# Performance work log

Measured on AMD Instinct MI355X. Metric: run time of the kernel, lower is better.

The kernel has to match this reference:

```python
import jax, jax.numpy as jnp
import numpy as np

B, E, D, P, H = 8192, 100, 300, 100, 20  # batch, experts, embed, projection, hidden

def setup_inputs() -> dict:
    key = jax.random.key(0)
    ks = jax.random.split(key, 10)
    return {
        "x": jax.random.normal(ks[0], (B, D), dtype=jnp.float32),
        "y": jax.random.normal(ks[1], (B, D), dtype=jnp.float32),
        "tag": jax.random.uniform(ks[2], (B, 1), dtype=jnp.float32),
        "weights_1": jax.random.normal(ks[3], (E, D, P), dtype=jnp.float32) * (2.0 / (D + P)) ** 0.5,
        "bias_1": jax.random.normal(ks[4], (E, P), dtype=jnp.float32) * 0.1,
        "hidden_weights": jax.random.normal(ks[5], (E, 2 * P + 2, H), dtype=jnp.float32) * 0.07,
        "hidden_bias": jax.random.normal(ks[6], (E, H), dtype=jnp.float32),
        "outlayer_weights": jax.random.normal(ks[7], (E, H, 1), dtype=jnp.float32) * 0.3,
        "outlayer_bias": jax.random.uniform(ks[8], (E, 1), dtype=jnp.float32),
        "weights_all": jax.random.normal(ks[9], (D, E), dtype=jnp.float32) * (2.0 / (D + E)) ** 0.5,
    }

def reference(x, y, tag, weights_1, bias_1, hidden_weights, hidden_bias,
              outlayer_weights, outlayer_bias, weights_all):
    eps = 1e-8
    # gating: softmax((x+y) @ W_all) over experts  -> [B, E, 1]
    w = jax.nn.softmax((x + y) @ weights_all, axis=1)[:, :, None]
    # per-expert projections: [B, E, P]
    xp = jnp.einsum('bd,edp->bep', x, weights_1) + bias_1
    yp = jnp.einsum('bd,edp->bep', y, weights_1) + bias_1
    # cosine similarity along projection dim (torch semantics: clamp each norm)
    nx = jnp.maximum(jnp.sqrt(jnp.sum(xp * xp, axis=2)), eps)
    ny = jnp.maximum(jnp.sqrt(jnp.sum(yp * yp, axis=2)), eps)
    cos = jnp.sum(xp * yp, axis=2) / (nx * ny)  # [B, E]
    tag_rep = jnp.broadcast_to(tag[:, None, :], (x.shape[0], weights_1.shape[0], tag.shape[1]))
    feat = jnp.concatenate([cos[:, :, None], xp + yp, jnp.abs(xp - yp), tag_rep], axis=2)  # [B,E,2P+2]
    h = jax.nn.relu(jnp.einsum('bef,efh->beh', feat, hidden_weights) + hidden_bias)  # [B,E,H]
    d = jnp.einsum('beh,eho->beo', h, outlayer_weights) + outlayer_bias  # [B,E,1]
    probs = jnp.squeeze(jnp.sum(w * d, axis=1), axis=-1)  # [B]
    return probs
```

## Files before the change

kernel.cpp:

```cpp
#include <hip/hip_runtime.h>
#include <math.h>

#define B_ 8192
#define E_ 100
#define D_ 300
#define P_ 100
#define H_ 20
#define F_ 202
#define NT 10
#define NWG 12800

typedef __attribute__((ext_vector_type(8))) short bf16x8;
typedef __attribute__((ext_vector_type(8))) _Float16 f16x8;
typedef __attribute__((ext_vector_type(4))) float f32x4;
typedef __attribute__((ext_vector_type(8))) unsigned short us8;

#define WG_OFF 0
#define AB_OFF 3276800
#define W1_OFF (AB_OFF + 20971520)
#define PD_OFF (W1_OFF + 14336000)
#define WS_NEEDED (PD_OFF + 3276800)

__device__ __forceinline__ unsigned short f2bf(float f) {
    unsigned int u = __float_as_uint(f);
    u = (u + 0x7FFF + ((u >> 16) & 1)) >> 16;
    return (unsigned short)u;
}
__device__ __forceinline__ float bf2f(unsigned short h) {
    return __uint_as_float(((unsigned int)h) << 16);
}

#define GLOAD16(g, l) \
    __builtin_amdgcn_global_load_lds((const __attribute__((address_space(1))) unsigned int*)(g), \
                                     (__attribute__((address_space(3))) unsigned int*)(l), 16, 0, 0)

__global__ __launch_bounds__(256) void prep_xy(const float* __restrict__ x,
                                               const float* __restrict__ y,
                                               unsigned short* __restrict__ ab2)
{
    const int bi = blockIdx.x;
    const int rb = bi / NT, t = bi - rb * NT;
    for (int s = threadIdx.x; s < 512; s += 256) {
        const int kg = s >> 7, row = s & 127;
        const float* src = ((row < 64) ? x : y) + (size_t)(rb * 64 + (row & 63)) * D_;
        const int k0 = t * 32 + kg * 8;
        us8 hi, lo;
        #pragma unroll
        for (int j = 0; j < 8; ++j) {
            const int k = k0 + j;
            const float v = (k < D_) ? src[k] : 0.f;
            const unsigned short h = f2bf(v);
            hi[j] = h;
            lo[j] = f2bf(v - bf2f(h));
        }
        unsigned short* tb = ab2 + (size_t)bi * 8192;
        *(us8*)(tb + (size_t)s * 8)         = hi;
        *(us8*)(tb + (size_t)(512 + s) * 8) = lo;
    }
}

__global__ __launch_bounds__(256) void prep_w1(const float* __restrict__ w1,
                                               unsigned short* __restrict__ w1b2)
{
    const int bi = blockIdx.x;
    const int e = bi / NT, t = bi - e * NT;
    for (int s = threadIdx.x; s < 448; s += 256) {
        const int kg = s / 112, p = s - kg * 112;
        const int k0 = t * 32 + kg * 8;
        us8 hi, lo;
        #pragma unroll
        for (int j = 0; j < 8; ++j) {
            const int k = k0 + j;
            const float v = (p < P_ && k < D_) ? w1[((size_t)e * D_ + k) * P_ + p] : 0.f;
            const unsigned short h = f2bf(v);
            hi[j] = h;
            lo[j] = f2bf(v - bf2f(h));
        }
        unsigned short* tb = w1b2 + (size_t)bi * 7168;
        *(us8*)(tb + (size_t)s * 8)         = hi;
        *(us8*)(tb + (size_t)(448 + s) * 8) = lo;
    }
}

__global__ __launch_bounds__(128) void gate_kernel(
    const float* __restrict__ x, const float* __restrict__ y,
    const float* __restrict__ wall, float* __restrict__ wgate)
{
    __shared__ float s[D_];
    __shared__ float zv[128];
    __shared__ float red[128];
    const int b = blockIdx.x;
    const int tid = threadIdx.x;

    for (int d = tid; d < D_; d += 128)
        s[d] = x[(size_t)b * D_ + d] + y[(size_t)b * D_ + d];
    __syncthreads();

    float acc = 0.f;
    if (tid < E_)
        for (int d = 0; d < D_; ++d) acc += s[d] * wall[(size_t)d * E_ + tid];
    zv[tid] = (tid < E_) ? acc : -INFINITY;
    red[tid] = zv[tid];
    __syncthreads();
    for (int st = 64; st > 0; st >>= 1) {
        if (tid < st) red[tid] = fmaxf(red[tid], red[tid + st]);
        __syncthreads();
    }
    const float m = red[0];
    __syncthreads();
    const float ev = (tid < E_) ? expf(zv[tid] - m) : 0.f;
    red[tid] = ev;
    __syncthreads();
    for (int st = 64; st > 0; st >>= 1) {
        if (tid < st) red[tid] += red[tid + st];
        __syncthreads();
    }
    if (tid < E_) wgate[(size_t)b * E_ + tid] = ev / red[0];
}

template<bool USE_PD>
__global__ __launch_bounds__(256, 3) void moe_mfma_kernel(
    const float* __restrict__ tag,
    const unsigned short* __restrict__ ab2,
    const unsigned short* __restrict__ w1b2,
    const float* __restrict__ b1,
    const float* __restrict__ wh,
    const float* __restrict__ hb,
    const float* __restrict__ wo,
    const float* __restrict__ ob,
    const float* __restrict__ wgate,
    float* __restrict__ pd,
    float* __restrict__ out)
{
    __shared__ __align__(16) char smem[48256];
    unsigned short (*Bw_lds)[7168] = (unsigned short (*)[7168])smem;
    _Float16 (*featl)[232] = (_Float16 (*)[232])smem;
    _Float16 (*swh2)[20][232] = (_Float16 (*)[20][232])(smem + 29696);

    const int tid  = threadIdx.x;
    const int lane = tid & 63, w = tid >> 6;

    const int bid = blockIdx.x;
    const int rb = ((bid & 7) << 4) | ((bid >> 3) & 15);
    const int e  = bid >> 7;
    const int b0 = rb * 64;
    const int li = lane & 15, kgq = lane >> 4;

    for (int k = tid; k < 20 * 232; k += 256) {
        const int h = k / 232, f = k - h * 232;
        const float v = (f < F_) ? wh[((size_t)e * F_ + f) * H_ + h] : 0.f;
        const _Float16 vh = (_Float16)v;
        (*swh2)[h][f] = vh;
        swh2[1][h][f] = (_Float16)(v - (float)vh);
    }

    f32x4 accx[7], accy[7];
    #pragma unroll
    for (int ni = 0; ni < 7; ++ni) {
        accx[ni] = (f32x4){0.f, 0.f, 0.f, 0.f};
        accy[ni] = (f32x4){0.f, 0.f, 0.f, 0.f};
    }

    const int a_base = (kgq * 128 + w * 16 + li) * 8;
    const int b_base = (kgq * 112 + li) * 8;

    bf16x8 areg[2][4];
    auto loadA = [&](int kt, int pb) {
        const unsigned short* tb = ab2 + (size_t)(rb * NT + kt) * 8192 + a_base;
        areg[pb][0] = *(const bf16x8*)(tb);
        areg[pb][1] = *(const bf16x8*)(tb + 4096);
        areg[pb][2] = *(const bf16x8*)(tb + 512);
        areg[pb][3] = *(const bf16x8*)(tb + 4608);
    };
    auto stageB = [&](int tt, int bb) {
        const unsigned short* bbase = w1b2 + (size_t)(e * NT + tt) * 7168 + lane * 8;
        #pragma unroll
        for (int k = 0; k < 4; ++k) {
            const int i = w + 4 * k;
            if (i < 14) GLOAD16(bbase + i * 512, &Bw_lds[bb][i * 512]);
        }
    };

    stageB(0, 0);
    loadA(0, 0);
    __syncthreads();
    #pragma unroll
    for (int kt = 0; kt < NT; ++kt) {
        const int cb = kt & 1, nb = cb ^ 1;
        if (kt < NT - 1) {
            stageB(kt + 1, nb);
            loadA(kt + 1, nb);
        }
        const bf16x8 axh = areg[cb][0];
        const bf16x8 axl = areg[cb][1];
        const bf16x8 ayh = areg[cb][2];
        const bf16x8 ayl = areg[cb][3];
        #pragma unroll
        for (int ni = 0; ni < 7; ++ni) {
            const bf16x8 bh = *(const bf16x8*)(&Bw_lds[cb][b_base + ni * 128]);
            const bf16x8 bl = *(const bf16x8*)(&Bw_lds[cb][b_base + ni * 128 + 3584]);
            accx[ni] = __builtin_amdgcn_mfma_f32_16x16x32_bf16(axh, bh, accx[ni], 0, 0, 0);
            accx[ni] = __builtin_amdgcn_mfma_f32_16x16x32_bf16(axl, bh, accx[ni], 0, 0, 0);
            accx[ni] = __builtin_amdgcn_mfma_f32_16x16x32_bf16(axh, bl, accx[ni], 0, 0, 0);
            accy[ni] = __builtin_amdgcn_mfma_f32_16x16x32_bf16(ayh, bh, accy[ni], 0, 0, 0);
            accy[ni] = __builtin_amdgcn_mfma_f32_16x16x32_bf16(ayl, bh, accy[ni], 0, 0, 0);
            accy[ni] = __builtin_amdgcn_mfma_f32_16x16x32_bf16(ayh, bl, accy[ni], 0, 0, 0);
        }
        __syncthreads();
    }

    for (int k = tid; k < 64 * 30; k += 256) featl[k / 30][202 + k % 30] = (_Float16)0.f;

    float pxx[4] = {0, 0, 0, 0}, pyy[4] = {0, 0, 0, 0}, pxy[4] = {0, 0, 0, 0};
    #pragma unroll
    for (int ni = 0; ni < 7; ++ni) {
        const int c = ni * 16 + li;
        if (c < P_) {
            const float bp = b1[(size_t)e * P_ + c];
            #pragma unroll
            for (int j = 0; j < 4; ++j) {
                const float xv = accx[ni][j] + bp;
                const float yv = accy[ni][j] + bp;
                const int r = w * 16 + kgq * 4 + j;
                featl[r][1 + c]   = (_Float16)(xv + yv);
                featl[r][101 + c] = (_Float16)fabsf(xv - yv);
                pxx[j] += xv * xv; pyy[j] += yv * yv; pxy[j] += xv * yv;
            }
        }
    }
    #pragma unroll
    for (int j = 0; j < 4; ++j) {
        #pragma unroll
        for (int m = 1; m < 16; m <<= 1) {
            pxx[j] += __shfl_xor(pxx[j], m);
            pyy[j] += __shfl_xor(pyy[j], m);
            pxy[j] += __shfl_xor(pxy[j], m);
        }
    }
    if (li == 0) {
        #pragma unroll
        for (int j = 0; j < 4; ++j) {
            const int r = w * 16 + kgq * 4 + j;
            const float nx = fmaxf(sqrtf(pxx[j]), 1e-8f);
            const float ny = fmaxf(sqrtf(pyy[j]), 1e-8f);
            featl[r][0]   = (_Float16)(pxy[j] / (nx * ny));
            featl[r][201] = (_Float16)tag[b0 + r];
        }
    }
    __syncthreads();

    const int h1 = 16 + li;
    const bool v1 = (h1 < H_);
    const int h1c = v1 ? h1 : (H_ - 1);

    f32x4 acc0 = (f32x4){0.f, 0.f, 0.f, 0.f};
    f32x4 acc1 = (f32x4){0.f, 0.f, 0.f, 0.f};
    #pragma unroll
    for (int kt = 0; kt < 7; ++kt) {
        const int ko = kt * 32 + kgq * 8;
        const f16x8 af  = *(const f16x8*)(&featl[w * 16 + li][ko]);
        const f16x8 b0h = *(const f16x8*)(&(*swh2)[li][ko]);
        const f16x8 b0l = *(const f16x8*)(&swh2[1][li][ko]);
        acc0 = __builtin_amdgcn_mfma_f32_16x16x32_f16(af, b0h, acc0, 0, 0, 0);
        acc0 = __builtin_amdgcn_mfma_f32_16x16x32_f16(af, b0l, acc0, 0, 0, 0);
        f16x8 b1h = *(const f16x8*)(&(*swh2)[h1c][ko]);
        f16x8 b1l = *(const f16x8*)(&swh2[1][h1c][ko]);
        if (!v1) {
            b1h = (f16x8)(_Float16)0.f;
            b1l = (f16x8)(_Float16)0.f;
        }
        acc1 = __builtin_amdgcn_mfma_f32_16x16x32_f16(af, b1h, acc1, 0, 0, 0);
        acc1 = __builtin_amdgcn_mfma_f32_16x16x32_f16(af, b1l, acc1, 0, 0, 0);
    }

    const float hb0 = hb[(size_t)e * H_ + li];
    const float wo0 = wo[(size_t)e * H_ + li];
    const float hb1 = v1 ? hb[(size_t)e * H_ + h1] : 0.f;
    const float wo1 = v1 ? wo[(size_t)e * H_ + h1] : 0.f;
    #pragma unroll
    for (int j = 0; j < 4; ++j) {
        float t = fmaxf(acc0[j] + hb0, 0.f) * wo0;
        if (v1) t += fmaxf(acc1[j] + hb1, 0.f) * wo1;
        t += __shfl_xor(t, 1);
        t += __shfl_xor(t, 2);
        t += __shfl_xor(t, 4);
        t += __shfl_xor(t, 8);
        if (li == 0) {
            const int r = w * 16 + kgq * 4 + j;
            const int b = b0 + r;
            const float v = wgate[(size_t)b * E_ + e] * (t + ob[e]);
            if (USE_PD) pd[(size_t)e * B_ + b] = v;
            else        atomicAdd(&out[b], v);
        }
    }
}

__global__ __launch_bounds__(256) void reduce_kernel(const float* __restrict__ pd,
                                                     float* __restrict__ out)
{
    const int b = blockIdx.x * 256 + threadIdx.x;
    float s = 0.f;
    for (int e = 0; e < E_; ++e) s += pd[(size_t)e * B_ + b];
    out[b] = s;
}

extern "C" void kernel_launch(void* const* d_in, const int* in_sizes, int n_in,
                              void* d_out, int out_size, void* d_ws, size_t ws_size,
                              hipStream_t stream)
{
    const float* x    = (const float*)d_in[0];
    const float* y    = (const float*)d_in[1];
    const float* tag  = (const float*)d_in[2];
    const float* w1   = (const float*)d_in[3];
    const float* b1   = (const float*)d_in[4];
    const float* wh   = (const float*)d_in[5];
    const float* hb   = (const float*)d_in[6];
    const float* wo   = (const float*)d_in[7];
    const float* ob   = (const float*)d_in[8];
    const float* wall = (const float*)d_in[9];

    float* out = (float*)d_out;
    char* ws = (char*)d_ws;
    float*          wgate = (float*)(ws + WG_OFF);
    unsigned short* ab2   = (unsigned short*)(ws + AB_OFF);
    unsigned short* w1b2  = (unsigned short*)(ws + W1_OFF);
    float*          pd    = (float*)(ws + PD_OFF);

    const bool use_pd = (ws_size >= (size_t)WS_NEEDED);

    prep_xy<<<dim3(128 * NT), dim3(256), 0, stream>>>(x, y, ab2);
    prep_w1<<<dim3(E_ * NT), dim3(256), 0, stream>>>(w1, w1b2);
    gate_kernel<<<dim3(B_), dim3(128), 0, stream>>>(x, y, wall, wgate);

    if (use_pd) {
        moe_mfma_kernel<true><<<dim3(NWG), dim3(256), 0, stream>>>(
            tag, ab2, w1b2, b1, wh, hb, wo, ob, wgate, pd, out);
        reduce_kernel<<<dim3(B_ / 256), dim3(256), 0, stream>>>(pd, out);
    } else {
        hipMemsetAsync(out, 0, (size_t)B_ * sizeof(float), stream);
        moe_mfma_kernel<false><<<dim3(NWG), dim3(256), 0, stream>>>(
            tag, ab2, w1b2, b1, wh, hb, wo, ob, wgate, pd, out);
    }
}
```

Measured before the change: 442.9 us.

## Precompute fp16 hidden weights globally and shrink LDS to raise occupancy

Adds a prep kernel that converts the hidden-layer weights into split fp16 hi/lo form once per expert in workspace, instead of every workgroup reconverting them into LDS. The main kernel in full-workspace mode then reads these B operands straight from global/L2, cutting its LDS footprint from about 48KB to 29.7KB and raising the launch-bounds occupancy hint from 3 to 5 waves. The trade-off is that the hidden-layer MFMA loop now issues global loads instead of LDS reads, and there is one extra kernel launch plus more workspace.

```diff
diff --git a/kernel.cpp b/kernel.cpp
--- a/kernel.cpp
+++ b/kernel.cpp
@@ -18,8 +18,10 @@
 #define WG_OFF 0
 #define AB_OFF 3276800
 #define W1_OFF (AB_OFF + 20971520)
-#define PD_OFF (W1_OFF + 14336000)
-#define WS_NEEDED (PD_OFF + 3276800)
+#define WH2_OFF (W1_OFF + 14336000)
+#define PD_OFF (WH2_OFF + 1856000)
+#define WS_ALL (PD_OFF + 3276800)
+#define WS_MIN (WH2_OFF)
 
 __device__ __forceinline__ unsigned short f2bf(float f) {
     unsigned int u = __float_as_uint(f);
@@ -82,6 +84,19 @@
     }
 }
 
+__global__ __launch_bounds__(256) void prep_wh(const float* __restrict__ wh,
+                                               _Float16* __restrict__ wh2)
+{
+    const int e = blockIdx.x;
+    for (int k = threadIdx.x; k < 20 * 232; k += 256) {
+        const int h = k / 232, f = k - h * 232;
+        const float v = (f < F_) ? wh[((size_t)e * F_ + f) * H_ + h] : 0.f;
+        const _Float16 vh = (_Float16)v;
+        wh2[(size_t)e * 9280 + k]        = vh;
+        wh2[(size_t)e * 9280 + 4640 + k] = (_Float16)(v - (float)vh);
+    }
+}
+
 __global__ __launch_bounds__(128) void gate_kernel(
     const float* __restrict__ x, const float* __restrict__ y,
     const float* __restrict__ wall, float* __restrict__ wgate)
@@ -118,11 +133,12 @@
     if (tid < E_) wgate[(size_t)b * E_ + tid] = ev / red[0];
 }
 
-template<bool USE_PD>
-__global__ __launch_bounds__(256, 3) void moe_mfma_kernel(
+template<int MODE>
+__global__ __launch_bounds__(256, (MODE == 1) ? 5 : 3) void moe_mfma_kernel(
     const float* __restrict__ tag,
     const unsigned short* __restrict__ ab2,
     const unsigned short* __restrict__ w1b2,
+    const _Float16* __restrict__ wh2g,
     const float* __restrict__ b1,
     const float* __restrict__ wh,
     const float* __restrict__ hb,
@@ -132,7 +148,7 @@
     float* __restrict__ pd,
     float* __restrict__ out)
 {
-    __shared__ __align__(16) char smem[48256];
+    __shared__ __align__(16) char smem[(MODE == 1) ? 29696 : 48256];
     unsigned short (*Bw_lds)[7168] = (unsigned short (*)[7168])smem;
     _Float16 (*featl)[232] = (_Float16 (*)[232])smem;
     _Float16 (*swh2)[20][232] = (_Float16 (*)[20][232])(smem + 29696);
@@ -146,12 +162,14 @@
     const int b0 = rb * 64;
     const int li = lane & 15, kgq = lane >> 4;
 
-    for (int k = tid; k < 20 * 232; k += 256) {
-        const int h = k / 232, f = k - h * 232;
-        const float v = (f < F_) ? wh[((size_t)e * F_ + f) * H_ + h] : 0.f;
-        const _Float16 vh = (_Float16)v;
-        (*swh2)[h][f] = vh;
-        swh2[1][h][f] = (_Float16)(v - (float)vh);
+    if constexpr (MODE == 0) {
+        for (int k = tid; k < 20 * 232; k += 256) {
+            const int h = k / 232, f = k - h * 232;
+            const float v = (f < F_) ? wh[((size_t)e * F_ + f) * H_ + h] : 0.f;
+            const _Float16 vh = (_Float16)v;
+            (*swh2)[h][f] = vh;
+            swh2[1][h][f] = (_Float16)(v - (float)vh);
+        }
     }
 
     f32x4 accx[7], accy[7];
@@ -252,23 +270,32 @@
     const int h1 = 16 + li;
     const bool v1 = (h1 < H_);
     const int h1c = v1 ? h1 : (H_ - 1);
+    const _Float16* whp = wh2g + (size_t)e * 9280;
 
     f32x4 acc0 = (f32x4){0.f, 0.f, 0.f, 0.f};
     f32x4 acc1 = (f32x4){0.f, 0.f, 0.f, 0.f};
     #pragma unroll
     for (int kt = 0; kt < 7; ++kt) {
         const int ko = kt * 32 + kgq * 8;
-        const f16x8 af  = *(const f16x8*)(&featl[w * 16 + li][ko]);
-        const f16x8 b0h = *(const f16x8*)(&(*swh2)[li][ko]);
-        const f16x8 b0l = *(const f16x8*)(&swh2[1][li][ko]);
-        acc0 = __builtin_amdgcn_mfma_f32_16x16x32_f16(af, b0h, acc0, 0, 0, 0);
-        acc0 = __builtin_amdgcn_mfma_f32_16x16x32_f16(af, b0l, acc0, 0, 0, 0);
-        f16x8 b1h = *(const f16x8*)(&(*swh2)[h1c][ko]);
-        f16x8 b1l = *(const f16x8*)(&swh2[1][h1c][ko]);
+        const f16x8 af = *(const f16x8*)(&featl[w * 16 + li][ko]);
+        f16x8 b0h, b0l, b1h, b1l;
+        if constexpr (MODE == 1) {
+            b0h = *(const f16x8*)(whp + li * 232 + ko);
+            b0l = *(const f16x8*)(whp + 4640 + li * 232 + ko);
+            b1h = *(const f16x8*)(whp + h1c * 232 + ko);
+            b1l = *(const f16x8*)(whp + 4640 + h1c * 232 + ko);
+        } else {
+            b0h = *(const f16x8*)(&(*swh2)[li][ko]);
+            b0l = *(const f16x8*)(&swh2[1][li][ko]);
+            b1h = *(const f16x8*)(&(*swh2)[h1c][ko]);
+            b1l = *(const f16x8*)(&swh2[1][h1c][ko]);
+        }
         if (!v1) {
             b1h = (f16x8)(_Float16)0.f;
             b1l = (f16x8)(_Float16)0.f;
         }
+        acc0 = __builtin_amdgcn_mfma_f32_16x16x32_f16(af, b0h, acc0, 0, 0, 0);
+        acc0 = __builtin_amdgcn_mfma_f32_16x16x32_f16(af, b0l, acc0, 0, 0, 0);
         acc1 = __builtin_amdgcn_mfma_f32_16x16x32_f16(af, b1h, acc1, 0, 0, 0);
         acc1 = __builtin_amdgcn_mfma_f32_16x16x32_f16(af, b1l, acc1, 0, 0, 0);
     }
@@ -289,8 +316,8 @@
             const int r = w * 16 + kgq * 4 + j;
             const int b = b0 + r;
             const float v = wgate[(size_t)b * E_ + e] * (t + ob[e]);
-            if (USE_PD) pd[(size_t)e * B_ + b] = v;
-            else        atomicAdd(&out[b], v);
+            if (MODE == 1) pd[(size_t)e * B_ + b] = v;
+            else           atomicAdd(&out[b], v);
         }
     }
 }
@@ -324,21 +351,23 @@
     float*          wgate = (float*)(ws + WG_OFF);
     unsigned short* ab2   = (unsigned short*)(ws + AB_OFF);
     unsigned short* w1b2  = (unsigned short*)(ws + W1_OFF);
+    _Float16*       wh2   = (_Float16*)(ws + WH2_OFF);
     float*          pd    = (float*)(ws + PD_OFF);
 
-    const bool use_pd = (ws_size >= (size_t)WS_NEEDED);
+    const bool full = (ws_size >= (size_t)WS_ALL);
 
     prep_xy<<<dim3(128 * NT), dim3(256), 0, stream>>>(x, y, ab2);
     prep_w1<<<dim3(E_ * NT), dim3(256), 0, stream>>>(w1, w1b2);
     gate_kernel<<<dim3(B_), dim3(128), 0, stream>>>(x, y, wall, wgate);
 
-    if (use_pd) {
-        moe_mfma_kernel<true><<<dim3(NWG), dim3(256), 0, stream>>>(
-            tag, ab2, w1b2, b1, wh, hb, wo, ob, wgate, pd, out);
+    if (full) {
+        prep_wh<<<dim3(E_), dim3(256), 0, stream>>>(wh, wh2);
+        moe_mfma_kernel<1><<<dim3(NWG), dim3(256), 0, stream>>>(
+            tag, ab2, w1b2, wh2, b1, wh, hb, wo, ob, wgate, pd, out);
         reduce_kernel<<<dim3(B_ / 256), dim3(256), 0, stream>>>(pd, out);
     } else {
         hipMemsetAsync(out, 0, (size_t)B_ * sizeof(float), stream);
-        moe_mfma_kernel<false><<<dim3(NWG), dim3(256), 0, stream>>>(
-            tag, ab2, w1b2, b1, wh, hb, wo, ob, wgate, pd, out);
-    }
-}
+        moe_mfma_kernel<0><<<dim3(NWG), dim3(256), 0, stream>>>(
+            tag, ab2, w1b2, wh2, b1, wh, hb, wo, ob, wgate, pd, out);
+    }
+}
```

Result: slower. 516.9 us (+16.7%).
